# Kernel optimization log

Measured on AMD Instinct MI355X. Metric: run time of the kernel, lower is better.

Reference implementation:

```python
import jax, jax.numpy as jnp
import numpy as np

# Llama-2-7B-like config with GQA
T, D, N, K, H = 2048, 4096, 32, 8, 128
THETA = 10000.0


def _rope(x, positions):
    """Split-ordering RoPE on last dim H of x: [..., T, heads, H]."""
    half = H // 2
    inv_freq = 1.0 / (THETA ** (jnp.arange(half, dtype=jnp.float32) / half))  # theta^(-2i/H)
    ang = positions.astype(jnp.float32)[:, None] * inv_freq[None, :]          # [T, half]
    cos = jnp.cos(ang)[:, None, :]
    sin = jnp.sin(ang)[:, None, :]
    x1, x2 = x[..., :half], x[..., half:]
    return jnp.concatenate([x1 * cos - x2 * sin, x2 * cos + x1 * sin], axis=-1).astype(x.dtype)


def setup_inputs() -> dict:
    key = jax.random.key(0)
    ks = jax.random.split(key, 5)
    s_in = 1.0 / np.sqrt(D)
    s_out = 1.0 / np.sqrt(N * H)
    return {
        "x": jax.random.normal(ks[0], (T, D), jnp.float32),
        "positions": jnp.arange(T, dtype=jnp.int32),
        "w_q": jax.random.normal(ks[1], (D, N, H), jnp.float32) * s_in,
        "w_k": jax.random.normal(ks[2], (D, K, H), jnp.float32) * s_in,
        "w_v": jax.random.normal(ks[3], (D, K, H), jnp.float32) * s_in,
        "w_o": jax.random.normal(ks[4], (N, H, D), jnp.float32) * s_out,
    }


def reference(x, positions, w_q, w_k, w_v, w_o):
    """Prefill path: fused QKV proj + RoPE + causal GQA attention + o_proj."""
    G = N // K  # query heads per kv head
    q = jnp.einsum('td,dnh->tnh', x, w_q)
    k = jnp.einsum('sd,dkh->skh', x, w_k)
    v = jnp.einsum('sd,dkh->skh', x, w_v)
    q = _rope(q, positions)
    k = _rope(k, positions)
    qg = q.reshape(T, K, G, H)
    scores = jnp.einsum('tkgh,skh->kgts', qg, k) * (H ** -0.5)
    causal = positions[:, None] >= positions[None, :]  # [T, S]
    scores = jnp.where(causal[None, None], scores, jnp.finfo(scores.dtype).min)
    probs = jax.nn.softmax(scores, axis=-1)
    out = jnp.einsum('kgts,skh->tkgh', probs, v).reshape(T, N, H)
    return jnp.einsum('tnh,nhd->td', out, w_o)
```

## Files before the change

### kernel.cpp

```cpp
#include <hip/hip_runtime.h>
#include <hip/hip_bf16.h>
#include <math.h>

#define T_SEQ   2048
#define D_MODEL 4096
#define N_Q     32
#define N_KV    8
#define HDIM    128
#define NH      (N_Q * HDIM)
#define KH      (N_KV * HDIM)
#define QKV_W   (NH + 2 * KH)

using bf16   = __hip_bfloat16;
using short8 = __attribute__((ext_vector_type(8))) short;
using floatx4 = __attribute__((ext_vector_type(4))) float;

__device__ __forceinline__ void load_lds16(const bf16* g, bf16* l) {
  __builtin_amdgcn_global_load_lds((const __attribute__((address_space(1))) void*)g,
                                   (__attribute__((address_space(3))) void*)l,
                                   16, 0, 0);
}

#define PB_CVT 2048
#define PB_SIN 2560
#define PB_WQ  3584
#define PB_WK  3840
#define PB_WV  4096
#define PB_WO  5120
__global__ __launch_bounds__(256)
void prep_all(const float* __restrict__ x, const int* __restrict__ pos,
              const float* __restrict__ w_q, const float* __restrict__ w_k,
              const float* __restrict__ w_v, const float* __restrict__ w_o,
              bf16* __restrict__ xb, float* __restrict__ ct, float* __restrict__ st,
              bf16* __restrict__ Bq, bf16* __restrict__ woT) {
  __shared__ __align__(16) bf16 tile[64][260];
  const int bid = blockIdx.x, tid = threadIdx.x;

  if (bid < PB_CVT) {
    const int base = bid * 256 + tid;
#pragma unroll
    for (int k = 0; k < 4; k++) {
      const int i = base + k * (PB_CVT * 256);
      const float4 v = ((const float4*)x)[i];
      union { bf16 h[4]; unsigned long long u; } o;
      o.h[0] = __float2bfloat16(v.x); o.h[1] = __float2bfloat16(v.y);
      o.h[2] = __float2bfloat16(v.z); o.h[3] = __float2bfloat16(v.w);
      ((unsigned long long*)xb)[i] = o.u;
    }
    return;
  }
  if (bid < PB_SIN) {
    const int i = (bid - PB_CVT) * 256 + tid;
    const int t = i >> 6, h = i & 63;
    const float p = (float)pos[t];
    const float inv = exp2f(-(float)h * 0.20762050592420985f);
    float s, c; sincosf(p * inv, &s, &c);
    ct[i] = c; st[i] = s;
    return;
  }
  const float* src; bf16* dst; int R, C, nx, local;
  if (bid < PB_WQ)      { local = bid - PB_SIN; src = w_q; dst = Bq;                               R = D_MODEL; C = NH; nx = 16; }
  else if (bid < PB_WK) { local = bid - PB_WQ;  src = w_k; dst = Bq + (size_t)NH * D_MODEL;        R = D_MODEL; C = KH; nx = 4; }
  else if (bid < PB_WV) { local = bid - PB_WK;  src = w_v; dst = Bq + (size_t)(NH + KH) * D_MODEL; R = D_MODEL; C = KH; nx = 4; }
  else                  { local = bid - PB_WV;  src = w_o; dst = woT;                              R = NH;      C = D_MODEL; nx = 16; }
  const int bx = (local % nx) * 256;
  const int by = (local / nx) * 64;
  const int cq = (tid & 63) * 4;
  const int rr = tid >> 6;
#pragma unroll
  for (int i = 0; i < 16; i++) {
    const int row = rr + i * 4;
    const float4 v = *(const float4*)&src[(size_t)(by + row) * C + bx + cq];
    union { bf16 h[4]; unsigned long long u; } o;
    o.h[0] = __float2bfloat16(v.x); o.h[1] = __float2bfloat16(v.y);
    o.h[2] = __float2bfloat16(v.z); o.h[3] = __float2bfloat16(v.w);
    *(unsigned long long*)&tile[row][cq] = o.u;
  }
  __syncthreads();
  const int ch  = (tid & 7) * 8;
  const int ocb = tid >> 3;
#pragma unroll
  for (int p2 = 0; p2 < 8; p2++) {
    const int oc = ocb + p2 * 32;
    union { bf16 h[8]; short8 s; } o;
#pragma unroll
    for (int j = 0; j < 8; j++) o.h[j] = tile[ch + j][oc];
    *(short8*)(dst + (size_t)(bx + oc) * R + by + ch) = o.s;
  }
}

__global__ __launch_bounds__(256)
void transpose_cvt(const float* __restrict__ src, bf16* __restrict__ dst, int R, int C) {
  __shared__ __align__(16) bf16 tile[64][260];
  const int bx = blockIdx.x * 256;
  const int by = blockIdx.y * 64;
  const int cq = (threadIdx.x & 63) * 4;
  const int rr = threadIdx.x >> 6;
#pragma unroll
  for (int i = 0; i < 16; i++) {
    const int row = rr + i * 4;
    const float4 v = *(const float4*)&src[(size_t)(by + row) * C + bx + cq];
    union { bf16 h[4]; unsigned long long u; } o;
    o.h[0] = __float2bfloat16(v.x); o.h[1] = __float2bfloat16(v.y);
    o.h[2] = __float2bfloat16(v.z); o.h[3] = __float2bfloat16(v.w);
    *(unsigned long long*)&tile[row][cq] = o.u;
  }
  __syncthreads();
  const int ch  = (threadIdx.x & 7) * 8;
  const int ocb = threadIdx.x >> 3;
#pragma unroll
  for (int p2 = 0; p2 < 8; p2++) {
    const int oc = ocb + p2 * 32;
    union { bf16 h[8]; short8 s; } o;
#pragma unroll
    for (int j = 0; j < 8; j++) o.h[j] = tile[ch + j][oc];
    *(short8*)(dst + (size_t)(bx + oc) * R + by + ch) = o.s;
  }
}

#define CS_STRIDE 137
template <int EPI>
__global__ __launch_bounds__(256)
void gemm_bt2(const bf16* __restrict__ A, const bf16* __restrict__ B,
              float* __restrict__ Cf, int N, int Kc, int hoff, int moff,
              const float* __restrict__ cosT, const float* __restrict__ sinT,
              bf16* __restrict__ Qo, bf16* __restrict__ Ko, bf16* __restrict__ Vo) {
  __shared__ bf16 smem[(EPI == 2) ? (128 * CS_STRIDE) : (128 * 128)];
  bf16* As = smem;
  bf16* Bs = smem + 128 * 64;

  const int tid  = threadIdx.x;
  const int lane = tid & 63;
  const int wave = tid >> 6;
  const int hy = blockIdx.y + hoff;
  const int bm = (blockIdx.x + moff) * 128;
  const int bn = hy * 128;
  const int wm = (wave >> 1) * 64;
  const int wn = (wave & 1) * 64;
  const int r = lane & 15, q = lane >> 4;

  floatx4 acc[4][4];
  const floatx4 zero = {0.f, 0.f, 0.f, 0.f};
#pragma unroll
  for (int i = 0; i < 4; i++)
#pragma unroll
    for (int j = 0; j < 4; j++) acc[i][j] = zero;

  const int rl = lane >> 3, ch = lane & 7;
  const int srow = wave * 32 + rl;
  const int gch = ch ^ rl;
  const bf16* gA = A + (size_t)(bm + srow) * Kc + gch * 8;
  const bf16* gB = B + (size_t)(bn + srow) * Kc + gch * 8;

  for (int k0 = 0; k0 < Kc; k0 += 64) {
    __syncthreads();
#pragma unroll
    for (int i = 0; i < 4; i++)
      load_lds16(gA + k0 + (size_t)i * 8 * Kc, As + (wave * 32 + i * 8) * 64);
#pragma unroll
    for (int i = 0; i < 4; i++)
      load_lds16(gB + k0 + (size_t)i * 8 * Kc, Bs + (wave * 32 + i * 8) * 64);
    __syncthreads();

#pragma unroll
    for (int ks = 0; ks < 2; ks++) {
      short8 af[4], bfr[4];
#pragma unroll
      for (int mt = 0; mt < 4; mt++)
        af[mt] = *(const short8*)(As + (wm + mt * 16 + r) * 64 + ((ks * 4 + q) ^ (r & 7)) * 8);
#pragma unroll
      for (int nt = 0; nt < 4; nt++)
        bfr[nt] = *(const short8*)(Bs + (wn + nt * 16 + r) * 64 + ((ks * 4 + q) ^ (r & 7)) * 8);
#pragma unroll
      for (int mt = 0; mt < 4; mt++)
#pragma unroll
        for (int nt = 0; nt < 4; nt++)
          acc[mt][nt] = __builtin_amdgcn_mfma_f32_16x16x32_bf16(af[mt], bfr[nt], acc[mt][nt], 0, 0, 0);
    }
  }

  if (EPI == 1) {
#pragma unroll
    for (int mt = 0; mt < 4; mt++)
#pragma unroll
      for (int nt = 0; nt < 4; nt++)
#pragma unroll
        for (int reg = 0; reg < 4; reg++) {
          const int row = bm + wm + mt * 16 + q * 4 + reg;
          const int col = bn + wn + nt * 16 + r;
          Cf[(size_t)row * N + col] = acc[mt][nt][reg];
        }
  } else {
    __syncthreads();
#pragma unroll
    for (int mt = 0; mt < 4; mt++)
#pragma unroll
      for (int nt = 0; nt < 4; nt++)
#pragma unroll
        for (int reg = 0; reg < 4; reg++)
          smem[(wm + mt * 16 + q * 4 + reg) * CS_STRIDE + wn + nt * 16 + r] =
              __float2bfloat16(acc[mt][nt][reg]);
    __syncthreads();

    const int hn = hy;
    if (hn < N_Q + N_KV) {
      const float SCL = 0.12751744868673310f;
      const bool isQ = (hn < N_Q);
      bf16* base = isQ ? (Qo + (size_t)bm * NH + hn * HDIM)
                       : (Ko + (size_t)bm * KH + (hn - N_Q) * HDIM);
      const int ostride = isQ ? NH : KH;
      for (int idx = tid; idx < 128 * 64; idx += 256) {
        const int row = idx >> 6, h = idx & 63;
        const float x1 = __bfloat162float(smem[row * CS_STRIDE + h]);
        const float x2 = __bfloat162float(smem[row * CS_STRIDE + h + 64]);
        const float cs = cosT[(bm + row) * 64 + h];
        const float sn = sinT[(bm + row) * 64 + h];
        float o1 = x1 * cs - x2 * sn;
        float o2 = x2 * cs + x1 * sn;
        if (isQ) { o1 *= SCL; o2 *= SCL; }
        bf16* d = base + (size_t)row * ostride;
        d[h]      = __float2bfloat16(o1);
        d[h + 64] = __float2bfloat16(o2);
      }
    } else {
      const int kh = hn - (N_Q + N_KV);
      for (int idx = tid; idx < 128 * 32; idx += 256) {
        const int h = idx >> 5, r4 = (idx & 31) * 4;
        union { bf16 h4[4]; unsigned long long u; } o;
#pragma unroll
        for (int j = 0; j < 4; j++) o.h4[j] = smem[(r4 + j) * CS_STRIDE + h];
        *(unsigned long long*)(Vo + ((size_t)kh * HDIM + h) * T_SEQ + bm + r4) = o.u;
      }
    }
  }
}

#define MSHIFT 8.0f
__global__ __launch_bounds__(256, 2)
void flash_attn(const bf16* __restrict__ Q, const bf16* __restrict__ Kk,
                const bf16* __restrict__ Vt, bf16* __restrict__ O) {
  const int id = blockIdx.x;
  const int n  = id & 31;
  const int kh = n >> 2;
  const int bt = (id < 256) ? (15 - (id >> 5)) : ((id - 256) >> 5);
  const int t0 = bt * 128;
  const int tid = threadIdx.x, lane = tid & 63, w = tid >> 6;
  const int r = lane & 15, q = lane >> 4;

  __shared__ bf16 Ks[64][128];
  __shared__ bf16 Vs[128][64];
  __shared__ bf16 Ps[4][32][72];

  short8 qf[2][4];
#pragma unroll
  for (int mf = 0; mf < 2; mf++) {
    const bf16* qrow = Q + (size_t)(t0 + w * 32 + mf * 16 + r) * NH + n * HDIM;
#pragma unroll
    for (int ks = 0; ks < 4; ks++)
      qf[mf][ks] = *(const short8*)(qrow + ks * 32 + q * 8);
  }

  floatx4 o_acc[2][8];
  const floatx4 zero = {0.f, 0.f, 0.f, 0.f};
#pragma unroll
  for (int mf = 0; mf < 2; mf++)
#pragma unroll
    for (int i = 0; i < 8; i++) o_acc[mf][i] = zero;
  float l_lane[2][4];
#pragma unroll
  for (int mf = 0; mf < 2; mf++)
#pragma unroll
    for (int i = 0; i < 4; i++) l_lane[mf][i] = 0.f;

  const int krl = lane >> 4, kc = lane & 15;
  const int vrl = lane >> 3, vc = lane & 7;

  short8 kr[4], vr[4];
#pragma unroll
  for (int i = 0; i < 4; i++) {
    const int row = (w * 4 + i) * 4 + krl;
    kr[i] = *(const short8*)(Kk + (size_t)row * KH + kh * HDIM + (kc ^ (row & 7)) * 8);
  }
#pragma unroll
  for (int i = 0; i < 4; i++) {
    const int row = (w * 4 + i) * 8 + vrl;
    vr[i] = *(const short8*)(Vt + ((size_t)(kh * HDIM + row)) * T_SEQ + (vc ^ (row & 7)) * 8);
  }

  const int nIter = 2 * bt + 2;
  for (int it = 0; it < nIter; ++it) {
    const int s0 = it * 64;
    __syncthreads();

#pragma unroll
    for (int i = 0; i < 4; i++)
      *(short8*)(&Ks[(w * 4 + i) * 4][0] + lane * 8) = kr[i];
#pragma unroll
    for (int i = 0; i < 4; i++)
      *(short8*)(&Vs[(w * 4 + i) * 8][0] + lane * 8) = vr[i];

    if (it + 1 < nIter) {
      const int s1 = s0 + 64;
#pragma unroll
      for (int i = 0; i < 4; i++) {
        const int row = (w * 4 + i) * 4 + krl;
        kr[i] = *(const short8*)(Kk + (size_t)(s1 + row) * KH + kh * HDIM + (kc ^ (row & 7)) * 8);
      }
#pragma unroll
      for (int i = 0; i < 4; i++) {
        const int row = (w * 4 + i) * 8 + vrl;
        vr[i] = *(const short8*)(Vt + ((size_t)(kh * HDIM + row)) * T_SEQ + s1 + (vc ^ (row & 7)) * 8);
      }
    }

    asm volatile("s_waitcnt lgkmcnt(0)" ::: "memory");
    __builtin_amdgcn_sched_barrier(0);
    __builtin_amdgcn_s_barrier();
    __builtin_amdgcn_sched_barrier(0);

    floatx4 sa[2][4];
#pragma unroll
    for (int mf = 0; mf < 2; mf++)
#pragma unroll
      for (int nt = 0; nt < 4; nt++) sa[mf][nt] = zero;
#pragma unroll
    for (int ks = 0; ks < 4; ks++)
#pragma unroll
      for (int nt = 0; nt < 4; nt++) {
        const int krow = nt * 16 + r;
        const short8 kb = *(const short8*)(&Ks[krow][(((ks * 4 + q) ^ (krow & 7))) * 8]);
#pragma unroll
        for (int mf = 0; mf < 2; mf++)
          sa[mf][nt] = __builtin_amdgcn_mfma_f32_16x16x32_bf16(qf[mf][ks], kb, sa[mf][nt], 0, 0, 0);
      }

#pragma unroll
    for (int mf = 0; mf < 2; mf++) {
      const int rbase = t0 + w * 32 + mf * 16;
      if (s0 + 63 > rbase) {
#pragma unroll
        for (int nt = 0; nt < 4; nt++)
#pragma unroll
          for (int reg = 0; reg < 4; reg++) {
            const int trow = rbase + q * 4 + reg;
            const int scol = s0 + nt * 16 + r;
            if (scol > trow) sa[mf][nt][reg] = -INFINITY;
          }
      }
#pragma unroll
      for (int nt = 0; nt < 4; nt++)
#pragma unroll
        for (int reg = 0; reg < 4; reg++) {
          const float p = exp2f(sa[mf][nt][reg] - MSHIFT);
          l_lane[mf][reg] += p;
          Ps[w][mf * 16 + q * 4 + reg][nt * 16 + r] = __float2bfloat16(p);
        }
    }

    __asm__ volatile("s_waitcnt lgkmcnt(0)" ::: "memory");

#pragma unroll
    for (int ks = 0; ks < 2; ks++) {
      short8 pa[2];
#pragma unroll
      for (int mf = 0; mf < 2; mf++)
        pa[mf] = *(const short8*)(&Ps[w][mf * 16 + r][ks * 32 + q * 8]);
#pragma unroll
      for (int ht = 0; ht < 8; ht++) {
        const int vrow = ht * 16 + r;
        const short8 vb = *(const short8*)(&Vs[vrow][(((ks * 4 + q) ^ (vrow & 7))) * 8]);
#pragma unroll
        for (int mf = 0; mf < 2; mf++)
          o_acc[mf][ht] = __builtin_amdgcn_mfma_f32_16x16x32_bf16(pa[mf], vb, o_acc[mf][ht], 0, 0, 0);
      }
    }
  }

#pragma unroll
  for (int mf = 0; mf < 2; mf++)
#pragma unroll
    for (int reg = 0; reg < 4; reg++) {
      float v = l_lane[mf][reg];
      v += __shfl_xor(v, 1); v += __shfl_xor(v, 2);
      v += __shfl_xor(v, 4); v += __shfl_xor(v, 8);
      const float inv_l = 1.0f / v;
      const int trow = t0 + w * 32 + mf * 16 + q * 4 + reg;
#pragma unroll
      for (int ht = 0; ht < 8; ht++)
        O[(size_t)trow * NH + n * HDIM + ht * 16 + r] =
            __float2bfloat16(o_acc[mf][ht][reg] * inv_l);
    }
}

extern "C" void kernel_launch(void* const* d_in, const int* in_sizes, int n_in,
                              void* d_out, int out_size, void* d_ws, size_t ws_size,
                              hipStream_t stream) {
  (void)in_sizes; (void)n_in; (void)out_size;
  const float* x   = (const float*)d_in[0];
  const int* pos   = (const int*)d_in[1];
  const float* w_q = (const float*)d_in[2];
  const float* w_k = (const float*)d_in[3];
  const float* w_v = (const float*)d_in[4];
  const float* w_o = (const float*)d_in[5];
  float* out = (float*)d_out;

  char* ws = (char*)d_ws;
  bf16*  xb   = (bf16*)(ws);
  bf16*  Bq   = (bf16*)(ws + (16ULL << 20));
  bf16*  Qr   = (bf16*)(ws + (64ULL << 20));
  bf16*  Kr   = (bf16*)(ws + (80ULL << 20));
  bf16*  Vt   = (bf16*)(ws + (84ULL << 20));
  bf16*  Oatt = (bf16*)(ws + (88ULL << 20));
  float* ct   = (float*)(ws + (104ULL << 20));
  float* st   = (float*)(ws + (105ULL << 20));

  const bool bigws = ws_size >= (138ULL << 20);
  bf16* woT = bigws ? (bf16*)(ws + (106ULL << 20)) : Bq;

  prep_all<<<bigws ? PB_WO : PB_WV, 256, 0, stream>>>(
      x, pos, w_q, w_k, w_v, w_o, xb, ct, st, Bq, woT);

  gemm_bt2<2><<<dim3(T_SEQ / 128, QKV_W / 128), 256, 0, stream>>>(
      xb, Bq, nullptr, QKV_W, D_MODEL, 0, 0, ct, st, Qr, Kr, Vt);

  if (!bigws)
    transpose_cvt<<<dim3(D_MODEL / 256, NH / 64), 256, 0, stream>>>(w_o, woT, NH, D_MODEL);

  flash_attn<<<dim3(512), 256, 0, stream>>>(Qr, Kr, Vt, Oatt);

  gemm_bt2<1><<<dim3(T_SEQ / 128, D_MODEL / 128), 256, 0, stream>>>(
      Oatt, woT, out, D_MODEL, NH, 0, 0, nullptr, nullptr, nullptr, nullptr, nullptr);
}
```

Before: 494.8 us.

## Replace QKV GEMM with 256x256-tile 8-wave ping-pong kernel using direct LDS loads

Adds a dedicated QKV projection kernel that computes a 256x256 output tile per 512-thread block instead of 128x128 per 256-thread block. It double-buffers A and B tiles in 128KB of LDS using global_load_lds with an XOR swizzle, and interleaves staging of the next k-tile with MFMA work through explicit barriers, waitcnts and s_setprio. The RoPE, scaling and V-transpose epilogue is adapted to handle two heads per block. The aim is better operand reuse and overlap of memory with compute. The cost is a much smaller grid (192 blocks), which may not fill all CUs, and only one block per CU because of the LDS footprint.

```diff
diff --git a/kernel.cpp b/kernel.cpp
--- a/kernel.cpp
+++ b/kernel.cpp
@@ -190,29 +190,129 @@
           const int col = bn + wn + nt * 16 + r;
           Cf[(size_t)row * N + col] = acc[mt][nt][reg];
         }
-  } else {
-    __syncthreads();
-#pragma unroll
-    for (int mt = 0; mt < 4; mt++)
-#pragma unroll
-      for (int nt = 0; nt < 4; nt++)
-#pragma unroll
-        for (int reg = 0; reg < 4; reg++)
-          smem[(wm + mt * 16 + q * 4 + reg) * CS_STRIDE + wn + nt * 16 + r] =
-              __float2bfloat16(acc[mt][nt][reg]);
-    __syncthreads();
-
-    const int hn = hy;
-    if (hn < N_Q + N_KV) {
-      const float SCL = 0.12751744868673310f;
+  }
+}
+
+#define A0_OFF 0
+#define B0_OFF 16384
+#define A1_OFF 32768
+#define B1_OFF 49152
+__global__ __launch_bounds__(512, 2)
+void gemm8p_qkv(const bf16* __restrict__ A, const bf16* __restrict__ B, int Kc,
+                const float* __restrict__ cosT, const float* __restrict__ sinT,
+                bf16* __restrict__ Qo, bf16* __restrict__ Ko, bf16* __restrict__ Vo) {
+  __shared__ __align__(16) bf16 smem[65536];
+  const int tid = threadIdx.x, lane = tid & 63, w = tid >> 6;
+  const int bm = blockIdx.x * 256, bn = blockIdx.y * 256;
+  const int wr = w >> 2, wc = w & 3;
+  const int r = lane & 15, q = lane >> 4;
+  const int rl = lane >> 3, ch = lane & 7;
+
+  const bf16* gA = A + (size_t)(bm + w * 16 + rl) * Kc + (ch ^ rl) * 8;
+  const bf16* gB = B + (size_t)(bn + w * 16 + rl) * Kc + (ch ^ rl) * 8;
+
+  floatx4 acc[8][4];
+  const floatx4 zero = {0.f, 0.f, 0.f, 0.f};
+#pragma unroll
+  for (int m = 0; m < 8; m++)
+#pragma unroll
+    for (int n = 0; n < 4; n++) acc[m][n] = zero;
+
+  short8 aT[4][2], bT0[2][2], bT1[2][2];
+
+#define STG_A(DOFF, H, KT)                                                        \
+  load_lds16(gA + (size_t)((H) * 128) * Kc + (KT),                                \
+             smem + (DOFF) + ((H) * 128 + w * 16) * 64);                          \
+  load_lds16(gA + (size_t)((H) * 128 + 8) * Kc + (KT),                            \
+             smem + (DOFF) + ((H) * 128 + w * 16 + 8) * 64);
+#define STG_B(DOFF, H, KT)                                                        \
+  load_lds16(gB + (size_t)((H) * 128) * Kc + (KT),                                \
+             smem + (DOFF) + ((H) * 128 + w * 16) * 64);                          \
+  load_lds16(gB + (size_t)((H) * 128 + 8) * Kc + (KT),                            \
+             smem + (DOFF) + ((H) * 128 + w * 16 + 8) * 64);
+#define RD_A8(OFF, MQ)                                                            \
+  _Pragma("unroll") for (int j = 0; j < 4; j++)                                   \
+  _Pragma("unroll") for (int ks = 0; ks < 2; ks++)                                \
+    aT[j][ks] = *(const short8*)(smem + (OFF) +                                   \
+        (wr * 128 + (MQ) * 64 + j * 16 + r) * 64 + ((ks * 4 + q) ^ (r & 7)) * 8);
+#define RD_B4(OFF, NQ, DSTB)                                                      \
+  _Pragma("unroll") for (int jn = 0; jn < 2; jn++)                                \
+  _Pragma("unroll") for (int ks = 0; ks < 2; ks++)                                \
+    DSTB[jn][ks] = *(const short8*)(smem + (OFF) +                                \
+        (wc * 64 + (NQ) * 32 + jn * 16 + r) * 64 + ((ks * 4 + q) ^ (r & 7)) * 8);
+#define MM16(MQ, NQ, BT)                                                          \
+  __builtin_amdgcn_s_setprio(1);                                                  \
+  _Pragma("unroll") for (int ks = 0; ks < 2; ks++)                                \
+  _Pragma("unroll") for (int j = 0; j < 4; j++)                                   \
+  _Pragma("unroll") for (int jn = 0; jn < 2; jn++)                                \
+    acc[(MQ) * 4 + j][(NQ) * 2 + jn] = __builtin_amdgcn_mfma_f32_16x16x32_bf16(   \
+        aT[j][ks], BT[jn][ks], acc[(MQ) * 4 + j][(NQ) * 2 + jn], 0, 0, 0);        \
+  __builtin_amdgcn_s_setprio(0);
+#define BAR __builtin_amdgcn_s_barrier()
+#define LGKM0 asm volatile("s_waitcnt lgkmcnt(0)" ::: "memory")
+#define VM4 asm volatile("s_waitcnt vmcnt(4)" ::: "memory")
+
+#define KTILE(CA, CB, DA, KA, DB, KB)                                             \
+  RD_A8(CA, 0); RD_B4(CB, 0, bT0);                                                \
+  STG_A(DA, 0, KA);                                                               \
+  BAR; LGKM0; MM16(0, 0, bT0); BAR;                                               \
+  RD_B4(CB, 1, bT1);                                                              \
+  STG_A(DA, 1, KA);                                                               \
+  BAR; LGKM0; MM16(0, 1, bT1); BAR;                                               \
+  RD_A8(CA, 1);                                                                   \
+  STG_B(DB, 0, KB);                                                               \
+  BAR; LGKM0; MM16(1, 1, bT1); BAR;                                               \
+  STG_B(DB, 1, KB);                                                               \
+  BAR; MM16(1, 0, bT0);                                                           \
+  VM4; BAR;
+
+  STG_A(A0_OFF, 0, 0); STG_A(A0_OFF, 1, 0);
+  STG_B(B0_OFF, 0, 0); STG_B(B0_OFF, 1, 0);
+  STG_B(B1_OFF, 0, 64); STG_B(B1_OFF, 1, 64);
+  VM4; BAR;
+
+  const int NT = Kc >> 6;
+  const int nIt = NT >> 1;
+  for (int i = 0; i < nIt; ++i) {
+    const int kb  = (2 * i + 1) * 64;
+    const int ka2 = (2 * i + 2 < NT) ? (2 * i + 2) * 64 : 0;
+    const int kb2 = (2 * i + 3 < NT) ? (2 * i + 3) * 64 : 0;
+    KTILE(A0_OFF, B0_OFF, A1_OFF, kb,  B0_OFF, ka2);
+    KTILE(A1_OFF, B1_OFF, A0_OFF, ka2, B1_OFF, kb2);
+  }
+#undef KTILE
+#undef STG_A
+#undef STG_B
+#undef RD_A8
+#undef RD_B4
+#undef MM16
+
+  asm volatile("s_waitcnt vmcnt(0)" ::: "memory");
+  BAR;
+#pragma unroll
+  for (int m = 0; m < 8; m++)
+#pragma unroll
+    for (int n = 0; n < 4; n++)
+#pragma unroll
+      for (int reg = 0; reg < 4; reg++)
+        smem[(wr * 128 + m * 16 + q * 4 + reg) * 256 + wc * 64 + n * 16 + r] =
+            __float2bfloat16(acc[m][n][reg]);
+  __syncthreads();
+
+  const int h0 = blockIdx.y * 2;
+  if (h0 < N_Q + N_KV) {
+    const float SCL = 0.12751744868673310f;
+#pragma unroll
+    for (int hh = 0; hh < 2; hh++) {
+      const int hn = h0 + hh;
       const bool isQ = (hn < N_Q);
       bf16* base = isQ ? (Qo + (size_t)bm * NH + hn * HDIM)
                        : (Ko + (size_t)bm * KH + (hn - N_Q) * HDIM);
       const int ostride = isQ ? NH : KH;
-      for (int idx = tid; idx < 128 * 64; idx += 256) {
+      for (int idx = tid; idx < 256 * 64; idx += 512) {
         const int row = idx >> 6, h = idx & 63;
-        const float x1 = __bfloat162float(smem[row * CS_STRIDE + h]);
-        const float x2 = __bfloat162float(smem[row * CS_STRIDE + h + 64]);
+        const float x1 = __bfloat162float(smem[row * 256 + hh * 128 + h]);
+        const float x2 = __bfloat162float(smem[row * 256 + hh * 128 + h + 64]);
         const float cs = cosT[(bm + row) * 64 + h];
         const float sn = sinT[(bm + row) * 64 + h];
         float o1 = x1 * cs - x2 * sn;
@@ -222,13 +322,16 @@
         d[h]      = __float2bfloat16(o1);
         d[h + 64] = __float2bfloat16(o2);
       }
-    } else {
-      const int kh = hn - (N_Q + N_KV);
-      for (int idx = tid; idx < 128 * 32; idx += 256) {
-        const int h = idx >> 5, r4 = (idx & 31) * 4;
+    }
+  } else {
+#pragma unroll
+    for (int hh = 0; hh < 2; hh++) {
+      const int kh = h0 + hh - (N_Q + N_KV);
+      for (int idx = tid; idx < 128 * 64; idx += 512) {
+        const int h = idx >> 6, r4 = (idx & 63) * 4;
         union { bf16 h4[4]; unsigned long long u; } o;
 #pragma unroll
-        for (int j = 0; j < 4; j++) o.h4[j] = smem[(r4 + j) * CS_STRIDE + h];
+        for (int j = 0; j < 4; j++) o.h4[j] = smem[(r4 + j) * 256 + hh * 128 + h];
         *(unsigned long long*)(Vo + ((size_t)kh * HDIM + h) * T_SEQ + bm + r4) = o.u;
       }
     }
@@ -420,8 +523,8 @@
   prep_all<<<bigws ? PB_WO : PB_WV, 256, 0, stream>>>(
       x, pos, w_q, w_k, w_v, w_o, xb, ct, st, Bq, woT);
 
-  gemm_bt2<2><<<dim3(T_SEQ / 128, QKV_W / 128), 256, 0, stream>>>(
-      xb, Bq, nullptr, QKV_W, D_MODEL, 0, 0, ct, st, Qr, Kr, Vt);
+  gemm8p_qkv<<<dim3(T_SEQ / 256, QKV_W / 256), 512, 0, stream>>>(
+      xb, Bq, D_MODEL, ct, st, Qr, Kr, Vt);
 
   if (!bigws)
     transpose_cvt<<<dim3(D_MODEL / 256, NH / 64), 256, 0, stream>>>(w_o, woT, NH, D_MODEL);
```

New measurement: 495.3 us. Within noise of the previous version (+0.1%).
